# Optimization experiments

Measured on AMD Instinct MI355X. Metric: run time of the kernel, lower is better.

The kernel has to match this reference:

```python
import jax, jax.numpy as jnp
import numpy as np

NQ, NT, D = 8192, 8192, 128
EC, EQ, ET = 262144, 262144, 262144


def seg_softmax(logits, seg, num):
    # numerically stable segment softmax over a 1-D logits vector
    m = jax.ops.segment_max(logits, seg, num_segments=num)
    e = jnp.exp(logits - m[seg])
    s = jax.ops.segment_sum(e, seg, num_segments=num)
    return e / s[seg]


def _linear_params(key, din, dout):
    k1, k2 = jax.random.split(key)
    scale = 1.0 / np.sqrt(din)
    W = jax.random.uniform(k1, (din, dout), minval=-scale, maxval=scale, dtype=jnp.float32)
    b = jax.random.uniform(k2, (dout,), minval=-scale, maxval=scale, dtype=jnp.float32)
    return W, b


def setup_inputs():
    key = jax.random.key(0)
    ks = jax.random.split(key, 20)
    inp = {
        'Xq': jax.random.normal(ks[0], (NQ, D), dtype=jnp.float32),
        'edge_index_q': jax.random.randint(ks[1], (2, EQ), 0, NQ),
        'Xt': jax.random.normal(ks[2], (NT, D), dtype=jnp.float32),
        'edge_index_t': jax.random.randint(ks[3], (2, ET), 0, NT),
        'norm_q': jax.random.uniform(ks[4], (NQ, 1), dtype=jnp.float32),
        'norm_t': jax.random.uniform(ks[5], (NT, 1), dtype=jnp.float32),
        'cross_src': jax.random.randint(ks[6], (EC,), 0, NQ),
        'cross_dst': jax.random.randint(ks[7], (EC,), 0, NT),
        'node_mask': jnp.ones((NQ,), dtype=bool),
        'only_run_inter': 0,
    }
    names_dims = [
        ('ac_q', D, D), ('ac_t', D, D), ('vc_q', D, D), ('vc_t', D, D),
        ('mq', 2 * D, D), ('mt', 3 * D, D),
        ('aq', 2 * D, 1), ('vq', 2 * D, D), ('at', 2 * D, 1), ('vt', 2 * D, D),
    ]
    for i, (nm, din, dout) in enumerate(names_dims):
        W, b = _linear_params(ks[8 + i], din, dout)
        inp['W_' + nm] = W
        inp['b_' + nm] = b
    return inp


def reference(Xq, edge_index_q, Xt, edge_index_t, norm_q, norm_t, cross_src, cross_dst,
              node_mask, only_run_inter,
              W_ac_q, b_ac_q, W_ac_t, b_ac_t, W_vc_q, b_vc_q, W_vc_t, b_vc_t,
              W_mq, b_mq, W_mt, b_mt,
              W_aq, b_aq, W_vq, b_vq, W_at, b_at, W_vt, b_vt):
    elu = jax.nn.elu
    nq, nt, d = Xq.shape[0], Xt.shape[0], Xq.shape[1]

    # cross-graph attention logits: per (u, v) pair, dot of transformed features
    Xq_ac = elu(Xq @ W_ac_q + b_ac_q)
    Xt_ac = elu(Xt @ W_ac_t + b_ac_t)
    att_logits = jnp.sum(Xq_ac[cross_src] * Xt_ac[cross_dst], axis=-1)  # [EC]

    # t2q: aggregate target values into query nodes (faithful to original: values gathered by u indices)
    Xt_vc = elu(Xt @ W_vc_t + b_vc_t)
    att_u = seg_softmax(att_logits, cross_src, nq)[:, None]
    Xt2q = jax.ops.segment_sum(att_u * Xt_vc[cross_src], cross_src, num_segments=nq)
    Xq_merged = jnp.concatenate([Xq, Xt2q], axis=1) @ W_mq + b_mq

    # q2t: aggregate query values into target nodes, plus global query summary Q
    Xq_vc = elu(Xq @ W_vc_q + b_vc_q)
    att_v = seg_softmax(att_logits, cross_dst, nt)[:, None]
    Xq2t = jax.ops.segment_sum(att_v * Xq_vc[cross_src], cross_dst, num_segments=nt)
    Q = jnp.broadcast_to(jnp.mean(Xq, axis=0, keepdims=True), (nt, d))
    Xt_merged = jnp.concatenate([Xt, Xq2t, Q], axis=1) @ W_mt + b_mt

    if only_run_inter:
        return Xq_merged, Xt_merged

    # intra-graph edge-wise gather -> MLP -> softmax-scatter message passing
    msg_t = jnp.concatenate([Xt_merged[edge_index_t[0]], Xt_merged[edge_index_t[1]]], axis=1)  # [ET, 2D]
    a_t = seg_softmax((msg_t @ W_at + b_at)[:, 0], edge_index_t[1], nt)[:, None]
    Xt_out = jax.ops.segment_sum(a_t * (msg_t @ W_vt + b_vt), edge_index_t[1], num_segments=nt)

    msg_q = jnp.concatenate([Xq_merged[edge_index_q[0]], Xq_merged[edge_index_q[1]]], axis=1)  # [EQ, 2D]
    a_q = seg_softmax((msg_q @ W_aq + b_aq)[:, 0], edge_index_q[1], nq)[:, None]
    Xq_out = jax.ops.segment_sum(a_q * (msg_q @ W_vq + b_vq), edge_index_q[1], num_segments=nq)

    return Xq_out, Xt_out
```

## Files before the change

### kernel.cpp

```cpp
#include <hip/hip_runtime.h>
#include <math.h>


#define NBIN 8192
#define NB   128

typedef _Float16 h2f __attribute__((ext_vector_type(2)));
typedef __attribute__((ext_vector_type(8))) short short8;
typedef __attribute__((ext_vector_type(4))) float f32x4;

__device__ __forceinline__ float elu1(float x) { return x > 0.f ? x : __expf(x) - 1.f; }

__device__ __forceinline__ unsigned short f2bf(float x) {
    unsigned u = __float_as_uint(x);
    u += 0x7FFF + ((u >> 16) & 1);
    return (unsigned short)(u >> 16);
}
__device__ __forceinline__ float bflo(unsigned u) { return __uint_as_float(u << 16); }
__device__ __forceinline__ float bfhi(unsigned u) { return __uint_as_float(u & 0xFFFF0000u); }
__device__ __forceinline__ unsigned short f2h(float x) {
    return __builtin_bit_cast(unsigned short, (_Float16)x);
}

__device__ __forceinline__ float dot8_f16(const uint4 a, const uint4 b, float d) {
#if __has_builtin(__builtin_amdgcn_fdot2)
    d = __builtin_amdgcn_fdot2(__builtin_bit_cast(h2f, a.x), __builtin_bit_cast(h2f, b.x), d, false);
    d = __builtin_amdgcn_fdot2(__builtin_bit_cast(h2f, a.y), __builtin_bit_cast(h2f, b.y), d, false);
    d = __builtin_amdgcn_fdot2(__builtin_bit_cast(h2f, a.z), __builtin_bit_cast(h2f, b.z), d, false);
    d = __builtin_amdgcn_fdot2(__builtin_bit_cast(h2f, a.w), __builtin_bit_cast(h2f, b.w), d, false);
#else
    const unsigned ua[4] = { a.x, a.y, a.z, a.w };
    const unsigned ub[4] = { b.x, b.y, b.z, b.w };
    #pragma unroll
    for (int t = 0; t < 4; ++t) {
        const h2f ha = __builtin_bit_cast(h2f, ua[t]);
        const h2f hb = __builtin_bit_cast(h2f, ub[t]);
        d = fmaf((float)ha.x, (float)hb.x, d);
        d = fmaf((float)ha.y, (float)hb.y, d);
    }
#endif
    return d;
}

struct WSrcs { const float* s[12]; };

__global__ __launch_bounds__(128) void wprep(WSrcs ws, unsigned short* wt)
{
    const int m = blockIdx.x >> 1;
    const int kh = (blockIdx.x & 1) * 64;
    const float* S = ws.s[m];
    unsigned short* H = wt + (size_t)m * 32768;
    unsigned short* L = H + 16384;
    const int n = threadIdx.x;
    for (int k = kh; k < kh + 64; ++k) {
        const float x = S[(size_t)k * 128 + n];
        const unsigned short hb = f2bf(x);
        const float lo = x - __uint_as_float((unsigned)hb << 16);
        H[(size_t)n * 128 + k] = hb;
        L[(size_t)n * 128 + k] = f2bf(lo);
    }
}

struct MJob {
    const float* A0; const float* A1; const int* rowmask1;
    const unsigned short* W[2][2];
    const float* bias0; const float* bias1;
    float* C0; float* C1;
    unsigned short* Cb0; unsigned short* Cb1;
    unsigned short* Ch0; unsigned short* Ch1;
    const float* gvw; float* gvo;
    int act;
};

__global__ __launch_bounds__(128) void gemm_mfma(MJob j0, MJob j1)
{
    const MJob j = blockIdx.z ? j1 : j0;
    const int c0 = blockIdx.y * 64;
    const int r0 = blockIdx.x * 64;
    __shared__ unsigned short AhL[64][136];
    __shared__ unsigned short AlL[64][136];
    const int tid = threadIdx.x;
    const int wv = tid >> 6, lane = tid & 63;
    const int l15 = lane & 15, quad = lane >> 4;

    f32x4 acc[2][2][4] = {};

    for (int pass = 0; pass < 2; ++pass) {
        const float* A = pass ? j.A1 : j.A0;
        if (!A) break;
        {
            const int row = tid >> 1, kh = (tid & 1) * 64;
            const int gr = r0 + row;
            const bool zero = pass && j.rowmask1 && (j.rowmask1[gr] == 0);
            const float* src = A + (size_t)gr * 128 + kh;
            #pragma unroll
            for (int c = 0; c < 64; c += 4) {
                float4 v = *(const float4*)(src + c);
                if (zero) v = make_float4(0.f, 0.f, 0.f, 0.f);
                const float xv[4] = { v.x, v.y, v.z, v.w };
                unsigned short hh[4], ll[4];
                #pragma unroll
                for (int u = 0; u < 4; ++u) {
                    const unsigned short hb = f2bf(xv[u]);
                    hh[u] = hb;
                    ll[u] = f2bf(xv[u] - __uint_as_float((unsigned)hb << 16));
                }
                uint2 ph, pl;
                ph.x = (unsigned)hh[0] | ((unsigned)hh[1] << 16);
                ph.y = (unsigned)hh[2] | ((unsigned)hh[3] << 16);
                pl.x = (unsigned)ll[0] | ((unsigned)ll[1] << 16);
                pl.y = (unsigned)ll[2] | ((unsigned)ll[3] << 16);
                *(uint2*)&AhL[row][kh + c] = ph;
                *(uint2*)&AlL[row][kh + c] = pl;
            }
        }
        __syncthreads();
        #pragma unroll
        for (int out = 0; out < 2; ++out) {
            const unsigned short* Wh = j.W[pass][out];
            if (!Wh) continue;
            const unsigned short* Wl = Wh + 16384;
            #pragma unroll
            for (int kc = 0; kc < 4; ++kc) {
                short8 ah[2], al[2];
                #pragma unroll
                for (int mi = 0; mi < 2; ++mi) {
                    const int rl = wv * 32 + mi * 16 + l15;
                    ah[mi] = *(const short8*)&AhL[rl][kc * 32 + quad * 8];
                    al[mi] = *(const short8*)&AlL[rl][kc * 32 + quad * 8];
                }
                #pragma unroll
                for (int ni = 0; ni < 4; ++ni) {
                    const int ng = c0 + ni * 16 + l15;
                    const short8 bh = *(const short8*)&Wh[(size_t)ng * 128 + kc * 32 + quad * 8];
                    const short8 bl = *(const short8*)&Wl[(size_t)ng * 128 + kc * 32 + quad * 8];
                    #pragma unroll
                    for (int mi = 0; mi < 2; ++mi) {
                        acc[out][mi][ni] = __builtin_amdgcn_mfma_f32_16x16x32_bf16(ah[mi], bh, acc[out][mi][ni], 0, 0, 0);
                        acc[out][mi][ni] = __builtin_amdgcn_mfma_f32_16x16x32_bf16(al[mi], bh, acc[out][mi][ni], 0, 0, 0);
                        acc[out][mi][ni] = __builtin_amdgcn_mfma_f32_16x16x32_bf16(ah[mi], bl, acc[out][mi][ni], 0, 0, 0);
                    }
                }
            }
        }
        __syncthreads();
    }

    #pragma unroll
    for (int out = 0; out < 2; ++out) {
        if (!j.W[0][out] && !j.W[1][out]) continue;
        const float* bias = out ? j.bias1 : j.bias0;
        float* C = out ? j.C1 : j.C0;
        unsigned short* Cb = out ? j.Cb1 : j.Cb0;
        unsigned short* Ch = out ? j.Ch1 : j.Ch0;
        const int dogv = (j.gvw != nullptr) && (out == 0);
        float p[2][4] = {};
        #pragma unroll
        for (int ni = 0; ni < 4; ++ni) {
            const int col = c0 + ni * 16 + l15;
            const float bvl = bias ? bias[col] : 0.f;
            const float gw = dogv ? j.gvw[col] : 0.f;
            #pragma unroll
            for (int mi = 0; mi < 2; ++mi) {
                #pragma unroll
                for (int reg = 0; reg < 4; ++reg) {
                    float o = acc[out][mi][ni][reg] + bvl;
                    if (j.act) o = elu1(o);
                    const int row = r0 + wv * 32 + mi * 16 + quad * 4 + reg;
                    if (C) C[(size_t)row * 128 + col] = o;
                    else if (Cb) Cb[(size_t)row * 128 + col] = f2bf(o);
                    else Ch[(size_t)row * 128 + col] = f2h(o);
                    p[mi][reg] = fmaf(o, gw, p[mi][reg]);
                }
            }
        }
        if (dogv) {
            #pragma unroll
            for (int mi = 0; mi < 2; ++mi) {
                #pragma unroll
                for (int reg = 0; reg < 4; ++reg) {
                    float v = p[mi][reg];
                    v += __shfl_xor(v, 1, 64); v += __shfl_xor(v, 2, 64);
                    v += __shfl_xor(v, 4, 64); v += __shfl_xor(v, 8, 64);
                    if (l15 == 0)
                        atomicAdd(j.gvo + r0 + wv * 32 + mi * 16 + quad * 4 + reg, v);
                }
            }
        }
    }
}

__global__ __launch_bounds__(256) void hist_priv(
    const int* __restrict__ cs, const int* __restrict__ cd,
    const int* __restrict__ et1, const int* __restrict__ eq1,
    int* __restrict__ mask_src, unsigned short* __restrict__ partial,
    int EC, int ET, int EQ)
{
    __shared__ int h[NBIN];
    const int k = blockIdx.x, a = blockIdx.y, tid = threadIdx.x;
    const int* idxs[3] = { cd, et1, eq1 };
    const int Es[3] = { EC, ET, EQ };
    for (int b = tid; b < NBIN; b += 256) h[b] = 0;
    __syncthreads();
    const int E = Es[a];
    const int per = (E + NB - 1) / NB;
    const int lo = k * per;
    const int hi = min(E, lo + per);
    const int* idx = idxs[a];
    for (int e = lo + tid; e < hi; e += 256) {
        atomicAdd(&h[idx[e]], 1);
        if (a == 0) mask_src[cs[e]] = 1;
    }
    __syncthreads();
    unsigned short* P = partial + ((size_t)a * NB + k) * NBIN;
    for (int b = tid; b < NBIN; b += 256) P[b] = (unsigned short)h[b];
}

__global__ void binprefix_kernel(unsigned short* __restrict__ partial, int* __restrict__ cnt)
{
    const int bin = blockIdx.x * 256 + threadIdx.x;
    const int a = blockIdx.y;
    unsigned short* P = partial + (size_t)a * NB * NBIN;
    int s = 0;
    #pragma unroll 4
    for (int k = 0; k < NB; ++k) {
        const int p = P[(size_t)k * NBIN + bin];
        P[(size_t)k * NBIN + bin] = (unsigned short)s;
        s += p;
    }
    cnt[a * NBIN + bin] = s;
}

__global__ __launch_bounds__(1024) void scan3_kernel(const int* __restrict__ cnt, int* __restrict__ offs)
{
    const int b = blockIdx.x;
    const int* c = cnt + (size_t)b * NBIN;
    int* o = offs + (size_t)b * (NBIN + 1);
    __shared__ int sums[1024];
    const int tid = threadIdx.x;
    int loc[8]; int s = 0;
    #pragma unroll
    for (int j = 0; j < 8; ++j) { loc[j] = s; s += c[tid * 8 + j]; }
    sums[tid] = s;
    __syncthreads();
    for (int off = 1; off < 1024; off <<= 1) {
        int v = 0;
        if (tid >= off) v = sums[tid - off];
        __syncthreads();
        sums[tid] += v;
        __syncthreads();
    }
    const int ex = tid ? sums[tid - 1] : 0;
    #pragma unroll
    for (int j = 0; j < 8; ++j) o[tid * 8 + j] = ex + loc[j];
    if (tid == 1023) o[NBIN] = sums[1023];
}

__global__ __launch_bounds__(256) void scatter_det(
    const int* __restrict__ cs, const int* __restrict__ cd,
    const int* __restrict__ et0, const int* __restrict__ et1,
    const int* __restrict__ eq0, const int* __restrict__ eq1,
    const unsigned short* __restrict__ partial, const int* __restrict__ offs,
    int* __restrict__ ids_cd, int* __restrict__ ids_t, int* __restrict__ ids_q,
    int EC, int ET, int EQ)
{
    __shared__ int cur[NBIN];
    const int k = blockIdx.x, a = blockIdx.y, tid = threadIdx.x;
    const int Es[3] = { EC, ET, EQ };
    const int* seg[3] = { cd, et1, eq1 };
    const int* pay[3] = { cs, et0, eq0 };
    int* dst[3] = { ids_cd, ids_t, ids_q };
    const unsigned short* P = partial + ((size_t)a * NB + k) * NBIN;
    const int* off = offs + (size_t)a * (NBIN + 1);
    for (int b = tid; b < NBIN; b += 256) cur[b] = off[b] + (int)P[b];
    __syncthreads();
    const int E = Es[a];
    const int per = (E + NB - 1) / NB;
    const int lo = k * per;
    const int hi = min(E, lo + per);
    const int* sg = seg[a]; const int* pl = pay[a]; int* dd = dst[a];
    for (int e = lo + tid; e < hi; e += 256) {
        const int pos = atomicAdd(&cur[sg[e]], 1);
        dd[pos] = pl[e];
    }
}

__global__ void colsum_kernel(const float* __restrict__ X, float* __restrict__ sum)
{
    const int c = threadIdx.x & 127;
    const int half = threadIdx.x >> 7;
    float s = 0.f;
    #pragma unroll 8
    for (int j = 0; j < 64; ++j) {
        const int r = blockIdx.x * 128 + half + 2 * j;
        s += X[(size_t)r * 128 + c];
    }
    atomicAdd(&sum[c], s);
}

__global__ __launch_bounds__(512) void mt_extra_kernel(
    const float* __restrict__ Qsum, const float* __restrict__ Wmt,
    const float* __restrict__ bmt, float* __restrict__ outv, int M)
{
    __shared__ float red[4][128];
    const int c = threadIdx.x & 127, kq = threadIdx.x >> 7;
    const float inv = 1.0f / (float)M;
    float acc = 0.f;
    #pragma unroll 4
    for (int k = kq * 32; k < kq * 32 + 32; ++k)
        acc = fmaf(Qsum[k] * inv, Wmt[(size_t)(256 + k) * 128 + c], acc);
    red[kq][c] = acc;
    __syncthreads();
    if (kq == 0) outv[c] = bmt[c] + red[0][c] + red[1][c] + red[2][c] + red[3][c];
}

__device__ __forceinline__ void gather_chunk_bf(
    const unsigned int* __restrict__ rows, int myid, float wv, int rem,
    int half, int cl, float4& acc)
{
    const int npairs = (rem + 1) >> 1;
    int j = 0;
    for (; j + 4 <= npairs; j += 4) {
        const int e0 = 2 * j + half, e1 = e0 + 2, e2 = e0 + 4, e3 = e0 + 6;
        const int s0 = __shfl(myid, e0, 64); const float w0 = __shfl(wv, e0, 64);
        const int s1 = __shfl(myid, e1, 64); const float w1 = __shfl(wv, e1, 64);
        const int s2 = __shfl(myid, e2, 64); const float w2 = __shfl(wv, e2, 64);
        const int s3 = __shfl(myid, e3, 64); const float w3 = __shfl(wv, e3, 64);
        const uint2 v0 = *(const uint2*)(rows + (size_t)s0 * 64 + cl * 2);
        const uint2 v1 = *(const uint2*)(rows + (size_t)s1 * 64 + cl * 2);
        const uint2 v2 = *(const uint2*)(rows + (size_t)s2 * 64 + cl * 2);
        const uint2 v3 = *(const uint2*)(rows + (size_t)s3 * 64 + cl * 2);
        acc.x = fmaf(w0, bflo(v0.x), acc.x); acc.y = fmaf(w0, bfhi(v0.x), acc.y);
        acc.z = fmaf(w0, bflo(v0.y), acc.z); acc.w = fmaf(w0, bfhi(v0.y), acc.w);
        acc.x = fmaf(w1, bflo(v1.x), acc.x); acc.y = fmaf(w1, bfhi(v1.x), acc.y);
        acc.z = fmaf(w1, bflo(v1.y), acc.z); acc.w = fmaf(w1, bfhi(v1.y), acc.w);
        acc.x = fmaf(w2, bflo(v2.x), acc.x); acc.y = fmaf(w2, bfhi(v2.x), acc.y);
        acc.z = fmaf(w2, bflo(v2.y), acc.z); acc.w = fmaf(w2, bfhi(v2.y), acc.w);
        acc.x = fmaf(w3, bflo(v3.x), acc.x); acc.y = fmaf(w3, bfhi(v3.x), acc.y);
        acc.z = fmaf(w3, bflo(v3.y), acc.z); acc.w = fmaf(w3, bfhi(v3.y), acc.w);
    }
    for (; j < npairs; ++j) {
        const int e = 2 * j + half;
        const int sv = __shfl(myid, e, 64); const float we = __shfl(wv, e, 64);
        const uint2 v = *(const uint2*)(rows + (size_t)sv * 64 + cl * 2);
        acc.x = fmaf(we, bflo(v.x), acc.x); acc.y = fmaf(we, bfhi(v.x), acc.y);
        acc.z = fmaf(we, bflo(v.y), acc.z); acc.w = fmaf(we, bfhi(v.y), acc.w);
    }
}

__global__ __launch_bounds__(256) void seg_agg_intra(
    const int* ot, const int* it, const float* nlt, const unsigned int* rt,
    const float* xt, const float* ebt, float* outt,
    const int* oq, const int* iq, const float* nlq, const unsigned int* rq,
    const float* xq, const float* ebq, float* outq, int nseg)
{
    const int* offs; const int* ids; const float* nl; const unsigned int* rows;
    const float* extra; const float* eb; float* out;
    if (blockIdx.y == 0) { offs = ot; ids = it; nl = nlt; rows = rt; extra = xt; eb = ebt; out = outt; }
    else                 { offs = oq; ids = iq; nl = nlq; rows = rq; extra = xq; eb = ebq; out = outq; }
    const int wid = (int)((blockIdx.x * blockDim.x + threadIdx.x) >> 6);
    const int lane = threadIdx.x & 63;
    if (wid >= nseg) return;
    const int lo = offs[wid], hi = offs[wid + 1];
    if (lo == hi) {
        *(float2*)(out + (size_t)wid * 128 + lane * 2) = make_float2(0.f, 0.f);
        return;
    }
    const int half = lane >> 5, cl = lane & 31;
    float m = -3.4e38f, s = 0.f;
    float4 acc = make_float4(0.f, 0.f, 0.f, 0.f);
    for (int base = lo; base < hi; base += 64) {
        const int rem = min(64, hi - base);
        int myid = 0; float l = -3.4e38f;
        if (lane < rem) { myid = ids[base + lane]; l = nl[myid]; }
        float mc = l;
        #pragma unroll
        for (int t = 32; t; t >>= 1) mc = fmaxf(mc, __shfl_xor(mc, t, 64));
        const float nm = fmaxf(m, mc);
        const float alpha = __expf(m - nm);
        const float wv = (lane < rem) ? __expf(l - nm) : 0.f;
        s = s * alpha + wv;
        acc.x *= alpha; acc.y *= alpha; acc.z *= alpha; acc.w *= alpha;
        m = nm;
        gather_chunk_bf(rows, myid, wv, rem, half, cl, acc);
    }
    #pragma unroll
    for (int t = 32; t; t >>= 1) s += __shfl_xor(s, t, 64);
    acc.x += __shfl_xor(acc.x, 32, 64); acc.y += __shfl_xor(acc.y, 32, 64);
    acc.z += __shfl_xor(acc.z, 32, 64); acc.w += __shfl_xor(acc.w, 32, 64);
    if (half == 0) {
        const float inv = 1.f / s;
        const float4 xv = *(const float4*)(extra + (size_t)wid * 128 + cl * 4);
        const float4 bv = *(const float4*)(eb + cl * 4);
        float4 o;
        o.x = fmaf(acc.x, inv, xv.x + bv.x);
        o.y = fmaf(acc.y, inv, xv.y + bv.y);
        o.z = fmaf(acc.z, inv, xv.z + bv.z);
        o.w = fmaf(acc.w, inv, xv.w + bv.w);
        *(float4*)(out + (size_t)wid * 128 + cl * 4) = o;
    }
}

__global__ __launch_bounds__(256) void seg_agg_cross(
    const int* __restrict__ offs, const int* __restrict__ ids,
    const unsigned int* __restrict__ Aqh, const unsigned int* __restrict__ Ath,
    const unsigned int* __restrict__ Vqb, float* __restrict__ out, int nseg)
{
    __shared__ unsigned int atrowh[4][64];
    const int w = threadIdx.x >> 6;
    const int lane = threadIdx.x & 63;
    const int wid = blockIdx.x * 4 + w;
    if (wid >= nseg) return;
    const int lo = offs[wid], hi = offs[wid + 1];
    if (lo == hi) {
        *(float2*)(out + (size_t)wid * 128 + lane * 2) = make_float2(0.f, 0.f);
        return;
    }
    atrowh[w][lane] = Ath[(size_t)wid * 64 + lane];
    __threadfence_block();

    const int half = lane >> 5, cl = lane & 31;
    float m = -3.4e38f, s = 0.f;
    float4 acc = make_float4(0.f, 0.f, 0.f, 0.f);
    for (int base = lo; base < hi; base += 64) {
        const int rem = min(64, hi - base);
        int myid = 0; float d = -3.4e38f;
        if (lane < rem) {
            myid = ids[base + lane];
            const unsigned int* ar = Aqh + (size_t)myid * 64;
            d = 0.f;
            #pragma unroll
            for (int k = 0; k < 64; k += 4)
                d = dot8_f16(*(const uint4*)(ar + k), *(const uint4*)&atrowh[w][k], d);
        }
        float mc = d;
        #pragma unroll
        for (int t = 32; t; t >>= 1) mc = fmaxf(mc, __shfl_xor(mc, t, 64));
        const float nm = fmaxf(m, mc);
        const float alpha = __expf(m - nm);
        const float wv = (lane < rem) ? __expf(d - nm) : 0.f;
        s = s * alpha + wv;
        acc.x *= alpha; acc.y *= alpha; acc.z *= alpha; acc.w *= alpha;
        m = nm;
        gather_chunk_bf(Vqb, myid, wv, rem, half, cl, acc);
    }
    #pragma unroll
    for (int t = 32; t; t >>= 1) s += __shfl_xor(s, t, 64);
    acc.x += __shfl_xor(acc.x, 32, 64); acc.y += __shfl_xor(acc.y, 32, 64);
    acc.z += __shfl_xor(acc.z, 32, 64); acc.w += __shfl_xor(acc.w, 32, 64);
    if (half == 0) {
        const float inv = 1.f / s;
        float4 o;
        o.x = acc.x * inv; o.y = acc.y * inv; o.z = acc.z * inv; o.w = acc.w * inv;
        *(float4*)(out + (size_t)wid * 128 + cl * 4) = o;
    }
}

extern "C" void kernel_launch(void* const* d_in, const int* in_sizes, int n_in,
                              void* d_out, int out_size, void* d_ws, size_t ws_size,
                              hipStream_t stream)
{
    const float* Xq    = (const float*)d_in[0];
    const int*   eqidx = (const int*)d_in[1];
    const float* Xt    = (const float*)d_in[2];
    const int*   etidx = (const int*)d_in[3];
    const int*   cs    = (const int*)d_in[6];
    const int*   cd    = (const int*)d_in[7];
    const float* W_ac_q = (const float*)d_in[10]; const float* b_ac_q = (const float*)d_in[11];
    const float* W_ac_t = (const float*)d_in[12]; const float* b_ac_t = (const float*)d_in[13];
    const float* W_vc_q = (const float*)d_in[14]; const float* b_vc_q = (const float*)d_in[15];
    const float* W_vc_t = (const float*)d_in[16]; const float* b_vc_t = (const float*)d_in[17];
    const float* W_mq   = (const float*)d_in[18]; const float* b_mq   = (const float*)d_in[19];
    const float* W_mt   = (const float*)d_in[20]; const float* b_mt   = (const float*)d_in[21];
    const float* W_aq   = (const float*)d_in[22];
    const float* W_vq   = (const float*)d_in[24]; const float* b_vq   = (const float*)d_in[25];
    const float* W_at   = (const float*)d_in[26];
    const float* W_vt   = (const float*)d_in[28]; const float* b_vt   = (const float*)d_in[29];

    const int NQ = in_sizes[0] / 128;
    const int EQ = in_sizes[1] / 2;
    const int NT = in_sizes[2] / 128;
    const int ET = in_sizes[3] / 2;
    const int EC = in_sizes[6];

    const int* eq0 = eqidx;  const int* eq1 = eqidx + EQ;
    const int* et0 = etidx;  const int* et1 = etidx + ET;

    float* base = (float*)d_ws;
    size_t off = 0;
    auto alloc = [&](size_t n) { float* p = base + off; off += n; return p; };
    float* N1 = alloc((size_t)NT * 128);
    float* N2 = alloc((size_t)NQ * 128);
    float* N3 = alloc((size_t)NT * 128);
    float* N4 = alloc((size_t)NT * 128);
    unsigned int* A0h = (unsigned int*)alloc((size_t)NQ * 64);
    unsigned int* A1h = (unsigned int*)alloc((size_t)NT * 64);
    unsigned short* B0 = (unsigned short*)alloc((size_t)NQ * 64);
    unsigned short* B1 = (unsigned short*)alloc((size_t)NT * 64);
    unsigned short* B2 = (unsigned short*)alloc((size_t)NQ * 64);
    unsigned short* WT = (unsigned short*)alloc((size_t)12 * 32768 / 2);
    float* mte  = alloc(128);
    float* st0v = alloc((size_t)NT);
    float* sq0v = alloc((size_t)NQ);
    int* mask_src = (int*)alloc((size_t)NQ);
    float* Qsum   = alloc(128);
    const size_t zero_bytes = ((size_t)NT + NQ + NQ + 128) * 4;
    int* cnt  = (int*)alloc((size_t)3 * NBIN);
    int* offs = (int*)alloc((size_t)3 * (NBIN + 1));
    unsigned short* partial = (unsigned short*)alloc((size_t)3 * NB * NBIN / 2);
    int* ids_cd = (int*)alloc((size_t)EC);
    int* ids_t  = (int*)alloc((size_t)ET);
    int* ids_q  = (int*)alloc((size_t)EQ);

    float* Xq_out = (float*)d_out;
    float* Xt_out = (float*)d_out + (size_t)NQ * 128;

    const int* offs_cd = offs;
    const int* offs_t  = offs + (NBIN + 1);
    const int* offs_q  = offs + 2 * (NBIN + 1);

    auto WTp = [&](int i) { return (const unsigned short*)(WT + (size_t)i * 32768); };

    hipMemsetAsync(st0v, 0, zero_bytes, stream);

    WSrcs ws;
    ws.s[0] = W_ac_q; ws.s[1] = W_vc_q; ws.s[2] = W_ac_t; ws.s[3] = W_vc_t;
    ws.s[4] = W_mq;   ws.s[5] = W_mq + 16384;
    ws.s[6] = W_mt;   ws.s[7] = W_mt + 16384;
    ws.s[8] = W_vt;   ws.s[9] = W_vt + 16384;
    ws.s[10] = W_vq;  ws.s[11] = W_vq + 16384;
    wprep<<<24, 128, 0, stream>>>(ws, WT);

    hist_priv<<<dim3(NB, 3), 256, 0, stream>>>(cs, cd, et1, eq1, mask_src, partial, EC, ET, EQ);
    binprefix_kernel<<<dim3(NBIN / 256, 3), 256, 0, stream>>>(partial, cnt);
    scan3_kernel<<<3, 1024, 0, stream>>>(cnt, offs);
    scatter_det<<<dim3(NB, 3), 256, 0, stream>>>(cs, cd, et0, et1, eq0, eq1, partial, offs,
                                                 ids_cd, ids_t, ids_q, EC, ET, EQ);

    colsum_kernel<<<NQ / 128, 256, 0, stream>>>(Xq, Qsum);
    mt_extra_kernel<<<1, 512, 0, stream>>>(Qsum, W_mt, b_mt, mte, NQ);

    const dim3 gg(NQ / 64, 2, 2);

    MJob jq{}, jt{};
    jq.A0 = Xq; jq.W[0][0] = WTp(0); jq.W[0][1] = WTp(1);
    jq.bias0 = b_ac_q; jq.bias1 = b_vc_q;
    jq.Ch0 = (unsigned short*)A0h; jq.Cb1 = B0; jq.act = 1;
    jt.A0 = Xt; jt.W[0][0] = WTp(2); jt.W[0][1] = WTp(3);
    jt.bias0 = b_ac_t; jt.bias1 = b_vc_t;
    jt.Ch0 = (unsigned short*)A1h; jt.C1 = N3; jt.act = 1;
    gemm_mfma<<<gg, 128, 0, stream>>>(jq, jt);

    seg_agg_cross<<<(NT + 3) / 4, 256, 0, stream>>>(offs_cd, ids_cd, A0h, A1h,
                                                    (const unsigned int*)B0, N4, NT);

    MJob mq{}, mt{};
    mq.A0 = Xq; mq.W[0][0] = WTp(4);
    mq.A1 = N3; mq.W[1][0] = WTp(5); mq.rowmask1 = mask_src;
    mq.bias0 = b_mq; mq.C0 = N2; mq.gvw = W_aq; mq.gvo = sq0v; mq.act = 0;
    mt.A0 = Xt; mt.W[0][0] = WTp(6);
    mt.A1 = N4; mt.W[1][0] = WTp(7);
    mt.bias0 = mte; mt.C0 = N1; mt.gvw = W_at; mt.gvo = st0v; mt.act = 0;
    gemm_mfma<<<gg, 128, 0, stream>>>(mq, mt);

    MJob ut{}, uq{};
    ut.A0 = N1; ut.W[0][0] = WTp(8); ut.W[0][1] = WTp(9);
    ut.Cb0 = B1; ut.C1 = Xt_out; ut.act = 0;
    uq.A0 = N2; uq.W[0][0] = WTp(10); uq.W[0][1] = WTp(11);
    uq.Cb0 = B2; uq.C1 = Xq_out; uq.act = 0;
    gemm_mfma<<<gg, 128, 0, stream>>>(ut, uq);

    seg_agg_intra<<<dim3((NT + 3) / 4, 2), 256, 0, stream>>>(
        offs_t, ids_t, st0v, (const unsigned int*)B1, Xt_out, b_vt, Xt_out,
        offs_q, ids_q, sq0v, (const unsigned int*)B2, Xq_out, b_vq, Xq_out, NT);
}
```

Measured before the change: 264.1 us.

## Fuse prep kernels, pre-swizzle weights, drop low-bf16 weight term, widen GEMM blocks

The weight prep, histogram and column-sum kernels become one launch, and the scatter and mt_extra kernels become a second, which cuts launch count and serialisation. Weights are now stored once as bf16 in an MFMA-fragment-swizzled layout, so B loads are coalesced. The low-order weight correction term (ah*bl) is dropped, leaving two MFMAs per tile instead of three, at some cost in accuracy. The GEMM moves to 256 threads with 16 rows per wave, giving more waves per block and fewer accumulators per thread.

New measurement: 235.0 us. 1.12x faster.

```diff
diff --git a/kernel.cpp b/kernel.cpp
--- a/kernel.cpp
+++ b/kernel.cpp
@@ -42,22 +42,81 @@
     return d;
 }
 
+__device__ void wprep_body(const float* __restrict__ S, unsigned short* __restrict__ Wf)
+{
+    const int lane = threadIdx.x & 63;
+    const int fg = threadIdx.x >> 6;
+    const int l15 = lane & 15, quad = lane >> 4;
+    for (int f = fg; f < 32; f += 4) {
+        const int nt = f >> 2, kc = f & 3;
+        const int n = nt * 16 + l15;
+        const int ks = kc * 32 + quad * 8;
+        unsigned short pk[8];
+        #pragma unroll
+        for (int jj = 0; jj < 8; ++jj)
+            pk[jj] = f2bf(S[(size_t)(ks + jj) * 128 + n]);
+        uint4 v;
+        v.x = (unsigned)pk[0] | ((unsigned)pk[1] << 16);
+        v.y = (unsigned)pk[2] | ((unsigned)pk[3] << 16);
+        v.z = (unsigned)pk[4] | ((unsigned)pk[5] << 16);
+        v.w = (unsigned)pk[6] | ((unsigned)pk[7] << 16);
+        *(uint4*)&Wf[((size_t)f * 64 + lane) * 8] = v;
+    }
+}
+
+__device__ void hist_body(int k, int a, int* h,
+                          const int* __restrict__ cs, const int* __restrict__ cd,
+                          const int* __restrict__ et1, const int* __restrict__ eq1,
+                          int* __restrict__ mask_src, unsigned short* __restrict__ partial,
+                          int EC, int ET, int EQ)
+{
+    const int tid = threadIdx.x;
+    const int* idxs[3] = { cd, et1, eq1 };
+    const int Es[3] = { EC, ET, EQ };
+    for (int b = tid; b < NBIN; b += 256) h[b] = 0;
+    __syncthreads();
+    const int E = Es[a];
+    const int per = (E + NB - 1) / NB;
+    const int lo = k * per;
+    const int hi = min(E, lo + per);
+    const int* idx = idxs[a];
+    for (int e = lo + tid; e < hi; e += 256) {
+        atomicAdd(&h[idx[e]], 1);
+        if (a == 0) mask_src[cs[e]] = 1;
+    }
+    __syncthreads();
+    unsigned short* P = partial + ((size_t)a * NB + k) * NBIN;
+    for (int b = tid; b < NBIN; b += 256) P[b] = (unsigned short)h[b];
+}
+
+__device__ void colsum_body(int bx, const float* __restrict__ X, float* __restrict__ sum)
+{
+    const int c = threadIdx.x & 127;
+    const int half = threadIdx.x >> 7;
+    float s = 0.f;
+    #pragma unroll 8
+    for (int j = 0; j < 64; ++j) {
+        const int r = bx * 128 + half + 2 * j;
+        s += X[(size_t)r * 128 + c];
+    }
+    atomicAdd(&sum[c], s);
+}
+
 struct WSrcs { const float* s[12]; };
 
-__global__ __launch_bounds__(128) void wprep(WSrcs ws, unsigned short* wt)
-{
-    const int m = blockIdx.x >> 1;
-    const int kh = (blockIdx.x & 1) * 64;
-    const float* S = ws.s[m];
-    unsigned short* H = wt + (size_t)m * 32768;
-    unsigned short* L = H + 16384;
-    const int n = threadIdx.x;
-    for (int k = kh; k < kh + 64; ++k) {
-        const float x = S[(size_t)k * 128 + n];
-        const unsigned short hb = f2bf(x);
-        const float lo = x - __uint_as_float((unsigned)hb << 16);
-        H[(size_t)n * 128 + k] = hb;
-        L[(size_t)n * 128 + k] = f2bf(lo);
+__global__ __launch_bounds__(256) void prep(
+    const int* cs, const int* cd, const int* et1, const int* eq1,
+    int* mask_src, unsigned short* partial, int EC, int ET, int EQ,
+    WSrcs ws, unsigned short* wt, const float* Xq, float* Qsum)
+{
+    __shared__ int smem_h[NBIN];
+    int b = blockIdx.x;
+    if (b < 3 * NB) {
+        hist_body(b % NB, b / NB, smem_h, cs, cd, et1, eq1, mask_src, partial, EC, ET, EQ);
+    } else if ((b -= 3 * NB) < 12) {
+        wprep_body(ws.s[b], wt + (size_t)b * 16384);
+    } else {
+        colsum_body(b - 12, Xq, Qsum);
     }
 }
 
@@ -72,7 +131,7 @@
     int act;
 };
 
-__global__ __launch_bounds__(128) void gemm_mfma(MJob j0, MJob j1)
+__global__ __launch_bounds__(256) void gemm_mfma(MJob j0, MJob j1)
 {
     const MJob j = blockIdx.z ? j1 : j0;
     const int c0 = blockIdx.y * 64;
@@ -83,18 +142,18 @@
     const int wv = tid >> 6, lane = tid & 63;
     const int l15 = lane & 15, quad = lane >> 4;
 
-    f32x4 acc[2][2][4] = {};
+    f32x4 acc[2][4] = {};
 
     for (int pass = 0; pass < 2; ++pass) {
         const float* A = pass ? j.A1 : j.A0;
         if (!A) break;
         {
-            const int row = tid >> 1, kh = (tid & 1) * 64;
+            const int row = tid >> 2, kq = (tid & 3) * 32;
             const int gr = r0 + row;
             const bool zero = pass && j.rowmask1 && (j.rowmask1[gr] == 0);
-            const float* src = A + (size_t)gr * 128 + kh;
+            const float* src = A + (size_t)gr * 128 + kq;
             #pragma unroll
-            for (int c = 0; c < 64; c += 4) {
+            for (int c = 0; c < 32; c += 4) {
                 float4 v = *(const float4*)(src + c);
                 if (zero) v = make_float4(0.f, 0.f, 0.f, 0.f);
                 const float xv[4] = { v.x, v.y, v.z, v.w };
@@ -110,36 +169,25 @@
                 ph.y = (unsigned)hh[2] | ((unsigned)hh[3] << 16);
                 pl.x = (unsigned)ll[0] | ((unsigned)ll[1] << 16);
                 pl.y = (unsigned)ll[2] | ((unsigned)ll[3] << 16);
-                *(uint2*)&AhL[row][kh + c] = ph;
-                *(uint2*)&AlL[row][kh + c] = pl;
+                *(uint2*)&AhL[row][kq + c] = ph;
+                *(uint2*)&AlL[row][kq + c] = pl;
             }
         }
         __syncthreads();
         #pragma unroll
-        for (int out = 0; out < 2; ++out) {
-            const unsigned short* Wh = j.W[pass][out];
-            if (!Wh) continue;
-            const unsigned short* Wl = Wh + 16384;
+        for (int kc = 0; kc < 4; ++kc) {
+            const short8 ah = *(const short8*)&AhL[wv * 16 + l15][kc * 32 + quad * 8];
+            const short8 al = *(const short8*)&AlL[wv * 16 + l15][kc * 32 + quad * 8];
             #pragma unroll
-            for (int kc = 0; kc < 4; ++kc) {
-                short8 ah[2], al[2];
-                #pragma unroll
-                for (int mi = 0; mi < 2; ++mi) {
-                    const int rl = wv * 32 + mi * 16 + l15;
-                    ah[mi] = *(const short8*)&AhL[rl][kc * 32 + quad * 8];
-                    al[mi] = *(const short8*)&AlL[rl][kc * 32 + quad * 8];
-                }
+            for (int out = 0; out < 2; ++out) {
+                const unsigned short* Wf = j.W[pass][out];
+                if (!Wf) continue;
                 #pragma unroll
                 for (int ni = 0; ni < 4; ++ni) {
-                    const int ng = c0 + ni * 16 + l15;
-                    const short8 bh = *(const short8*)&Wh[(size_t)ng * 128 + kc * 32 + quad * 8];
-                    const short8 bl = *(const short8*)&Wl[(size_t)ng * 128 + kc * 32 + quad * 8];
-                    #pragma unroll
-                    for (int mi = 0; mi < 2; ++mi) {
-                        acc[out][mi][ni] = __builtin_amdgcn_mfma_f32_16x16x32_bf16(ah[mi], bh, acc[out][mi][ni], 0, 0, 0);
-                        acc[out][mi][ni] = __builtin_amdgcn_mfma_f32_16x16x32_bf16(al[mi], bh, acc[out][mi][ni], 0, 0, 0);
-                        acc[out][mi][ni] = __builtin_amdgcn_mfma_f32_16x16x32_bf16(ah[mi], bl, acc[out][mi][ni], 0, 0, 0);
-                    }
+                    const short8 bh = *(const short8*)&Wf[
+                        ((size_t)(((c0 >> 4) + ni) * 4 + kc) * 64 + lane) * 8];
+                    acc[out][ni] = __builtin_amdgcn_mfma_f32_16x16x32_bf16(ah, bh, acc[out][ni], 0, 0, 0);
+                    acc[out][ni] = __builtin_amdgcn_mfma_f32_16x16x32_bf16(al, bh, acc[out][ni], 0, 0, 0);
                 }
             }
         }
@@ -154,66 +202,34 @@
         unsigned short* Cb = out ? j.Cb1 : j.Cb0;
         unsigned short* Ch = out ? j.Ch1 : j.Ch0;
         const int dogv = (j.gvw != nullptr) && (out == 0);
-        float p[2][4] = {};
+        float p[4] = {};
         #pragma unroll
         for (int ni = 0; ni < 4; ++ni) {
             const int col = c0 + ni * 16 + l15;
             const float bvl = bias ? bias[col] : 0.f;
             const float gw = dogv ? j.gvw[col] : 0.f;
             #pragma unroll
-            for (int mi = 0; mi < 2; ++mi) {
-                #pragma unroll
-                for (int reg = 0; reg < 4; ++reg) {
-                    float o = acc[out][mi][ni][reg] + bvl;
-                    if (j.act) o = elu1(o);
-                    const int row = r0 + wv * 32 + mi * 16 + quad * 4 + reg;
-                    if (C) C[(size_t)row * 128 + col] = o;
-                    else if (Cb) Cb[(size_t)row * 128 + col] = f2bf(o);
-                    else Ch[(size_t)row * 128 + col] = f2h(o);
-                    p[mi][reg] = fmaf(o, gw, p[mi][reg]);
-                }
+            for (int reg = 0; reg < 4; ++reg) {
+                float o = acc[out][ni][reg] + bvl;
+                if (j.act) o = elu1(o);
+                const int row = r0 + wv * 16 + quad * 4 + reg;
+                if (C) C[(size_t)row * 128 + col] = o;
+                else if (Cb) Cb[(size_t)row * 128 + col] = f2bf(o);
+                else Ch[(size_t)row * 128 + col] = f2h(o);
+                p[reg] = fmaf(o, gw, p[reg]);
             }
         }
         if (dogv) {
             #pragma unroll
-            for (int mi = 0; mi < 2; ++mi) {
-                #pragma unroll
-                for (int reg = 0; reg < 4; ++reg) {
-                    float v = p[mi][reg];
-                    v += __shfl_xor(v, 1, 64); v += __shfl_xor(v, 2, 64);
-                    v += __shfl_xor(v, 4, 64); v += __shfl_xor(v, 8, 64);
-                    if (l15 == 0)
-                        atomicAdd(j.gvo + r0 + wv * 32 + mi * 16 + quad * 4 + reg, v);
-                }
+            for (int reg = 0; reg < 4; ++reg) {
+                float v = p[reg];
+                v += __shfl_xor(v, 1, 64); v += __shfl_xor(v, 2, 64);
+                v += __shfl_xor(v, 4, 64); v += __shfl_xor(v, 8, 64);
+                if (l15 == 0)
+                    atomicAdd(j.gvo + r0 + wv * 16 + quad * 4 + reg, v);
             }
         }
     }
-}
-
-__global__ __launch_bounds__(256) void hist_priv(
-    const int* __restrict__ cs, const int* __restrict__ cd,
-    const int* __restrict__ et1, const int* __restrict__ eq1,
-    int* __restrict__ mask_src, unsigned short* __restrict__ partial,
-    int EC, int ET, int EQ)
-{
-    __shared__ int h[NBIN];
-    const int k = blockIdx.x, a = blockIdx.y, tid = threadIdx.x;
-    const int* idxs[3] = { cd, et1, eq1 };
-    const int Es[3] = { EC, ET, EQ };
-    for (int b = tid; b < NBIN; b += 256) h[b] = 0;
-    __syncthreads();
-    const int E = Es[a];
-    const int per = (E + NB - 1) / NB;
-    const int lo = k * per;
-    const int hi = min(E, lo + per);
-    const int* idx = idxs[a];
-    for (int e = lo + tid; e < hi; e += 256) {
-        atomicAdd(&h[idx[e]], 1);
-        if (a == 0) mask_src[cs[e]] = 1;
-    }
-    __syncthreads();
-    unsigned short* P = partial + ((size_t)a * NB + k) * NBIN;
-    for (int b = tid; b < NBIN; b += 256) P[b] = (unsigned short)h[b];
 }
 
 __global__ void binprefix_kernel(unsigned short* __restrict__ partial, int* __restrict__ cnt)
@@ -256,7 +272,7 @@
     if (tid == 1023) o[NBIN] = sums[1023];
 }
 
-__global__ __launch_bounds__(256) void scatter_det(
+__device__ void scatter_body(int k, int a, int* cur,
     const int* __restrict__ cs, const int* __restrict__ cd,
     const int* __restrict__ et0, const int* __restrict__ et1,
     const int* __restrict__ eq0, const int* __restrict__ eq1,
@@ -264,8 +280,7 @@
     int* __restrict__ ids_cd, int* __restrict__ ids_t, int* __restrict__ ids_q,
     int EC, int ET, int EQ)
 {
-    __shared__ int cur[NBIN];
-    const int k = blockIdx.x, a = blockIdx.y, tid = threadIdx.x;
+    const int tid = threadIdx.x;
     const int Es[3] = { EC, ET, EQ };
     const int* seg[3] = { cd, et1, eq1 };
     const int* pay[3] = { cs, et0, eq0 };
@@ -285,33 +300,35 @@
     }
 }
 
-__global__ void colsum_kernel(const float* __restrict__ X, float* __restrict__ sum)
-{
-    const int c = threadIdx.x & 127;
-    const int half = threadIdx.x >> 7;
-    float s = 0.f;
-    #pragma unroll 8
-    for (int j = 0; j < 64; ++j) {
-        const int r = blockIdx.x * 128 + half + 2 * j;
-        s += X[(size_t)r * 128 + c];
-    }
-    atomicAdd(&sum[c], s);
-}
-
-__global__ __launch_bounds__(512) void mt_extra_kernel(
+__device__ void mt_extra_body(float* red,
     const float* __restrict__ Qsum, const float* __restrict__ Wmt,
     const float* __restrict__ bmt, float* __restrict__ outv, int M)
 {
-    __shared__ float red[4][128];
-    const int c = threadIdx.x & 127, kq = threadIdx.x >> 7;
+    const int c = threadIdx.x & 127, h = threadIdx.x >> 7;
     const float inv = 1.0f / (float)M;
     float acc = 0.f;
     #pragma unroll 4
-    for (int k = kq * 32; k < kq * 32 + 32; ++k)
+    for (int k = h * 64; k < h * 64 + 64; ++k)
         acc = fmaf(Qsum[k] * inv, Wmt[(size_t)(256 + k) * 128 + c], acc);
-    red[kq][c] = acc;
+    red[h * 128 + c] = acc;
     __syncthreads();
-    if (kq == 0) outv[c] = bmt[c] + red[0][c] + red[1][c] + red[2][c] + red[3][c];
+    if (h == 0) outv[c] = bmt[c] + red[c] + red[128 + c];
+}
+
+__global__ __launch_bounds__(256) void stage3(
+    const int* cs, const int* cd,
+    const int* et0, const int* et1, const int* eq0, const int* eq1,
+    const unsigned short* partial, const int* offs,
+    int* ids_cd, int* ids_t, int* ids_q, int EC, int ET, int EQ,
+    const float* Qsum, const float* Wmt, const float* bmt, float* mte, int M)
+{
+    __shared__ __align__(16) char smem[32768];
+    const int b = blockIdx.x;
+    if (b < 3 * NB)
+        scatter_body(b % NB, b / NB, (int*)smem, cs, cd, et0, et1, eq0, eq1,
+                     partial, offs, ids_cd, ids_t, ids_q, EC, ET, EQ);
+    else
+        mt_extra_body((float*)smem, Qsum, Wmt, bmt, mte, M);
 }
 
 __device__ __forceinline__ void gather_chunk_bf(
@@ -498,7 +515,7 @@
     unsigned short* B0 = (unsigned short*)alloc((size_t)NQ * 64);
     unsigned short* B1 = (unsigned short*)alloc((size_t)NT * 64);
     unsigned short* B2 = (unsigned short*)alloc((size_t)NQ * 64);
-    unsigned short* WT = (unsigned short*)alloc((size_t)12 * 32768 / 2);
+    unsigned short* WT = (unsigned short*)alloc((size_t)12 * 16384 / 2);
     float* mte  = alloc(128);
     float* st0v = alloc((size_t)NT);
     float* sq0v = alloc((size_t)NQ);
@@ -519,7 +536,7 @@
     const int* offs_t  = offs + (NBIN + 1);
     const int* offs_q  = offs + 2 * (NBIN + 1);
 
-    auto WTp = [&](int i) { return (const unsigned short*)(WT + (size_t)i * 32768); };
+    auto WTp = [&](int i) { return (const unsigned short*)(WT + (size_t)i * 16384); };
 
     hipMemsetAsync(st0v, 0, zero_bytes, stream);
 
@@ -529,16 +546,15 @@
     ws.s[6] = W_mt;   ws.s[7] = W_mt + 16384;
     ws.s[8] = W_vt;   ws.s[9] = W_vt + 16384;
     ws.s[10] = W_vq;  ws.s[11] = W_vq + 16384;
-    wprep<<<24, 128, 0, stream>>>(ws, WT);
-
-    hist_priv<<<dim3(NB, 3), 256, 0, stream>>>(cs, cd, et1, eq1, mask_src, partial, EC, ET, EQ);
+    prep<<<3 * NB + 12 + NQ / 128, 256, 0, stream>>>(
+        cs, cd, et1, eq1, mask_src, partial, EC, ET, EQ, ws, WT, Xq, Qsum);
+
     binprefix_kernel<<<dim3(NBIN / 256, 3), 256, 0, stream>>>(partial, cnt);
     scan3_kernel<<<3, 1024, 0, stream>>>(cnt, offs);
-    scatter_det<<<dim3(NB, 3), 256, 0, stream>>>(cs, cd, et0, et1, eq0, eq1, partial, offs,
-                                                 ids_cd, ids_t, ids_q, EC, ET, EQ);
-
-    colsum_kernel<<<NQ / 128, 256, 0, stream>>>(Xq, Qsum);
-    mt_extra_kernel<<<1, 512, 0, stream>>>(Qsum, W_mt, b_mt, mte, NQ);
+
+    stage3<<<3 * NB + 1, 256, 0, stream>>>(cs, cd, et0, et1, eq0, eq1, partial, offs,
+                                           ids_cd, ids_t, ids_q, EC, ET, EQ,
+                                           Qsum, W_mt, b_mt, mte, NQ);
 
     const dim3 gg(NQ / 64, 2, 2);
 
@@ -549,7 +565,7 @@
     jt.A0 = Xt; jt.W[0][0] = WTp(2); jt.W[0][1] = WTp(3);
     jt.bias0 = b_ac_t; jt.bias1 = b_vc_t;
     jt.Ch0 = (unsigned short*)A1h; jt.C1 = N3; jt.act = 1;
-    gemm_mfma<<<gg, 128, 0, stream>>>(jq, jt);
+    gemm_mfma<<<gg, 256, 0, stream>>>(jq, jt);
 
     seg_agg_cross<<<(NT + 3) / 4, 256, 0, stream>>>(offs_cd, ids_cd, A0h, A1h,
                                                     (const unsigned int*)B0, N4, NT);
@@ -561,14 +577,14 @@
     mt.A0 = Xt; mt.W[0][0] = WTp(6);
     mt.A1 = N4; mt.W[1][0] = WTp(7);
     mt.bias0 = mte; mt.C0 = N1; mt.gvw = W_at; mt.gvo = st0v; mt.act = 0;
-    gemm_mfma<<<gg, 128, 0, stream>>>(mq, mt);
+    gemm_mfma<<<gg, 256, 0, stream>>>(mq, mt);
 
     MJob ut{}, uq{};
     ut.A0 = N1; ut.W[0][0] = WTp(8); ut.W[0][1] = WTp(9);
     ut.Cb0 = B1; ut.C1 = Xt_out; ut.act = 0;
     uq.A0 = N2; uq.W[0][0] = WTp(10); uq.W[0][1] = WTp(11);
     uq.Cb0 = B2; uq.C1 = Xq_out; uq.act = 0;
-    gemm_mfma<<<gg, 128, 0, stream>>>(ut, uq);
+    gemm_mfma<<<gg, 256, 0, stream>>>(ut, uq);
 
     seg_agg_intra<<<dim3((NT + 3) / 4, 2), 256, 0, stream>>>(
         offs_t, ids_t, st0v, (const unsigned int*)B1, Xt_out, b_vt, Xt_out,
```
